# Optimization experiments

Hardware: AMD Instinct MI355X
Metric: run time of the kernel (lower is better)

## Reference

```python
import jax, jax.numpy as jnp
import numpy as np

D_MODEL = 1024
NUM_HEADS = 16
D_HEAD = D_MODEL // NUM_HEADS


def setup_inputs() -> dict:
    key = jax.random.key(0)
    ks = jax.random.split(key, 12)
    B, S = 4, 2048
    scale = 1.0 / np.sqrt(D_MODEL)
    inp = {
        "query": jax.random.normal(ks[0], (B, S, D_MODEL), dtype=jnp.float32),
        "key": jax.random.normal(ks[1], (B, S, D_MODEL), dtype=jnp.float32),
        "value": jax.random.normal(ks[2], (B, S, D_MODEL), dtype=jnp.float32),
        "Wq": jax.random.normal(ks[3], (D_MODEL, D_MODEL), dtype=jnp.float32) * scale,
        "bq": jnp.zeros((D_MODEL,), dtype=jnp.float32),
        "Wk": jax.random.normal(ks[4], (D_MODEL, D_MODEL), dtype=jnp.float32) * scale,
        "bk": jnp.zeros((D_MODEL,), dtype=jnp.float32),
        "Wv": jax.random.normal(ks[5], (D_MODEL, D_MODEL), dtype=jnp.float32) * scale,
        "bv": jnp.zeros((D_MODEL,), dtype=jnp.float32),
        "Wo": jax.random.normal(ks[6], (D_MODEL, D_MODEL), dtype=jnp.float32) * scale,
        "bo": jnp.zeros((D_MODEL,), dtype=jnp.float32),
    }
    return inp


def reference(query, key, value, Wq, bq, Wk, bk, Wv, bv, Wo, bo):
    B, S, _ = query.shape
    # Linear projections (torch Linear: x @ W.T + b), split into heads: [B, H, S, Dh]
    Q = (query @ Wq.T + bq).reshape(B, S, NUM_HEADS, D_HEAD).transpose(0, 2, 1, 3)
    K = (key @ Wk.T + bk).reshape(B, S, NUM_HEADS, D_HEAD).transpose(0, 2, 1, 3)
    V = (value @ Wv.T + bv).reshape(B, S, NUM_HEADS, D_HEAD).transpose(0, 2, 1, 3)
    scores = jnp.einsum("bhqd,bhkd->bhqk", Q, K) / np.sqrt(D_HEAD).astype(np.float32)
    attn = jax.nn.softmax(scores, axis=-1)  # dropout is identity in eval mode
    out = jnp.einsum("bhqk,bhkd->bhqd", attn, V)
    out = out.transpose(0, 2, 1, 3).reshape(B, S, D_MODEL)
    out = out @ Wo.T + bo
    avg_attention = attn.mean(axis=1)  # [B, S, S]
    return (out, avg_attention)
```

## Files before the change

### kernel.cpp

```cpp
#include <hip/hip_runtime.h>
#include <hip/hip_bf16.h>


#define DEVI __device__ __forceinline__

typedef __attribute__((ext_vector_type(8))) short bf16x8;
typedef __attribute__((ext_vector_type(4))) float f32x4;

#define MFMA_BF16(a, b, c) __builtin_amdgcn_mfma_f32_16x16x32_bf16(a, b, c, 0, 0, 0)

constexpr int Bn = 4;
constexpr int Sn = 2048;
constexpr int Dn = 1024;
constexpr int Hn = 16;

DEVI unsigned short f2bf_rn(float x) {
    unsigned u = __float_as_uint(x);
    u += 0x7fffu + ((u >> 16) & 1u);
    return (unsigned short)(u >> 16);
}
DEVI float bf2f(unsigned short h) { return __uint_as_float(((unsigned)h) << 16); }

DEVI int swz32(int r, int k) { return r * 32 + ((((k >> 3) ^ r) & 3) << 3) + (k & 7); }
DEVI int swz64(int r, int k) { return r * 64 + ((((k >> 3) ^ r) & 7) << 3) + (k & 7); }

DEVI void gload16(const unsigned short* g, unsigned short* l) {
    __builtin_amdgcn_global_load_lds(
        (const __attribute__((address_space(1))) unsigned int*)g,
        (__attribute__((address_space(3))) unsigned int*)l, 16, 0, 0);
}

__global__ __launch_bounds__(256) void cvt_plain3(
    const float* __restrict__ a, const float* __restrict__ b, const float* __restrict__ c,
    unsigned short* __restrict__ oa, unsigned short* __restrict__ ob,
    unsigned short* __restrict__ oc)
{
    const float* s = blockIdx.y == 0 ? a : blockIdx.y == 1 ? b : c;
    unsigned short* d = blockIdx.y == 0 ? oa : blockIdx.y == 1 ? ob : oc;
    const size_t i = ((size_t)blockIdx.x * 256 + threadIdx.x) * 8;
    const float4 v0 = *reinterpret_cast<const float4*>(s + i);
    const float4 v1 = *reinterpret_cast<const float4*>(s + i + 4);
    const float* p0 = reinterpret_cast<const float*>(&v0);
    const float* p1 = reinterpret_cast<const float*>(&v1);
    bf16x8 o;
#pragma unroll
    for (int j = 0; j < 4; ++j) {
        o[j] = (short)f2bf_rn(p0[j]);
        o[4 + j] = (short)f2bf_rn(p1[j]);
    }
    *reinterpret_cast<bf16x8*>(d + i) = o;
}

__global__ __launch_bounds__(256) void cvt_split4(
    const float* __restrict__ w0, const float* __restrict__ w1,
    const float* __restrict__ w2, const float* __restrict__ w3,
    unsigned short* __restrict__ h0, unsigned short* __restrict__ l0,
    unsigned short* __restrict__ h1, unsigned short* __restrict__ l1,
    unsigned short* __restrict__ h2, unsigned short* __restrict__ l2,
    unsigned short* __restrict__ h3, unsigned short* __restrict__ l3)
{
    const int y = blockIdx.y;
    const float* s = y == 0 ? w0 : y == 1 ? w1 : y == 2 ? w2 : w3;
    unsigned short* dh = y == 0 ? h0 : y == 1 ? h1 : y == 2 ? h2 : h3;
    unsigned short* dl = y == 0 ? l0 : y == 1 ? l1 : y == 2 ? l2 : l3;
    const size_t i = ((size_t)blockIdx.x * 256 + threadIdx.x) * 8;
    const float4 v0 = *reinterpret_cast<const float4*>(s + i);
    const float4 v1 = *reinterpret_cast<const float4*>(s + i + 4);
    const float* p0 = reinterpret_cast<const float*>(&v0);
    const float* p1 = reinterpret_cast<const float*>(&v1);
    bf16x8 oh, ol;
#pragma unroll
    for (int j = 0; j < 4; ++j) {
        unsigned short h = f2bf_rn(p0[j]);
        oh[j] = (short)h;
        ol[j] = (short)f2bf_rn(p0[j] - bf2f(h));
        h = f2bf_rn(p1[j]);
        oh[4 + j] = (short)h;
        ol[4 + j] = (short)f2bf_rn(p1[j] - bf2f(h));
    }
    *reinterpret_cast<bf16x8*>(dh + i) = oh;
    *reinterpret_cast<bf16x8*>(dl + i) = ol;
}

template <int MODE>
__global__ __launch_bounds__(256) void gemm_bf(
    const unsigned short* __restrict__ Xbf,
    const unsigned short* __restrict__ Whi, const unsigned short* __restrict__ Wlo,
    const float* __restrict__ bias, float oscale,
    unsigned short* __restrict__ o_bf, float* __restrict__ o_f32)
{
    constexpr int K = Dn;
    __shared__ __align__(16) unsigned short sA[128 * 32];
    __shared__ __align__(16) unsigned short sBh[128 * 32];
    __shared__ __align__(16) unsigned short sBl[128 * 32];

    const int tid = threadIdx.x, lane = tid & 63, w = tid >> 6;
    const int row0 = blockIdx.y * 128, col0 = blockIdx.x * 128;
    const int wm = (w >> 1) * 64, wn = (w & 1) * 64;
    const int fr = lane & 15, hi = lane >> 4, kof = hi * 8;

    const int g0 = tid, g1 = tid + 256;
    const int r0 = g0 >> 2, c0 = ((g0 & 3) ^ r0) & 3;
    const int r1 = g1 >> 2, c1 = ((g1 & 3) ^ r1) & 3;

    const unsigned short* pa0 = Xbf + (size_t)(row0 + r0) * K + c0 * 8;
    const unsigned short* pa1 = Xbf + (size_t)(row0 + r1) * K + c1 * 8;
    const unsigned short* pbh0 = Whi + (size_t)(col0 + r0) * K + c0 * 8;
    const unsigned short* pbh1 = Whi + (size_t)(col0 + r1) * K + c1 * 8;
    const unsigned short* pbl0 = Wlo + (size_t)(col0 + r0) * K + c0 * 8;
    const unsigned short* pbl1 = Wlo + (size_t)(col0 + r1) * K + c1 * 8;

    f32x4 acc[4][4] = {};

    for (int k0 = 0; k0 < K; k0 += 32) {
        gload16(pa0 + k0, &sA[(w * 64) * 8]);
        gload16(pa1 + k0, &sA[(256 + w * 64) * 8]);
        gload16(pbh0 + k0, &sBh[(w * 64) * 8]);
        gload16(pbh1 + k0, &sBh[(256 + w * 64) * 8]);
        gload16(pbl0 + k0, &sBl[(w * 64) * 8]);
        gload16(pbl1 + k0, &sBl[(256 + w * 64) * 8]);
        __syncthreads();

        bf16x8 fa[4], fbh[4], fbl[4];
#pragma unroll
        for (int m = 0; m < 4; ++m) fa[m] = *(const bf16x8*)&sA[swz32(wm + m * 16 + fr, kof)];
#pragma unroll
        for (int n = 0; n < 4; ++n) {
            const int ib = swz32(wn + n * 16 + fr, kof);
            fbh[n] = *(const bf16x8*)&sBh[ib];
            fbl[n] = *(const bf16x8*)&sBl[ib];
        }
#pragma unroll
        for (int m = 0; m < 4; ++m)
#pragma unroll
            for (int n = 0; n < 4; ++n) {
                acc[m][n] = MFMA_BF16(fa[m], fbh[n], acc[m][n]);
                acc[m][n] = MFMA_BF16(fa[m], fbl[n], acc[m][n]);
            }
        __syncthreads();
    }

    float bv_[4];
#pragma unroll
    for (int n = 0; n < 4; ++n) bv_[n] = bias[col0 + wn + n * 16 + fr];

#pragma unroll
    for (int m = 0; m < 4; ++m)
#pragma unroll
        for (int n = 0; n < 4; ++n)
#pragma unroll
            for (int r = 0; r < 4; ++r) {
                const int row = row0 + wm + m * 16 + hi * 4 + r;
                const int col = col0 + wn + n * 16 + fr;
                float v = acc[m][n][r] + bv_[n];
                if (MODE == 0) {
                    v *= oscale;
                    const int bb = row >> 11, s = row & 2047;
                    const int hh = col >> 6, dh = col & 63;
                    o_bf[((size_t)(bb * Hn + hh) * Sn + s) * 64 + dh] = f2bf_rn(v);
                } else if (MODE == 1) {
                    const int bb = row >> 11, s = row & 2047;
                    const int hh = col >> 6, dh = col & 63;
                    o_bf[((size_t)(bb * Hn + hh) * 64 + dh) * Sn + s] = f2bf_rn(v);
                } else {
                    o_f32[(size_t)row * Dn + col] = v;
                }
            }
}

__global__ __launch_bounds__(256) void flash_fwd(
    const unsigned short* __restrict__ Qbf, const unsigned short* __restrict__ Kbf,
    const unsigned short* __restrict__ Vt,
    unsigned short* __restrict__ attn_bf, float* __restrict__ m_ws, float* __restrict__ l_ws)
{
    __shared__ __align__(16) unsigned short kh_l[2][64 * 64];
    __shared__ __align__(16) unsigned short vt_l[2][64 * 64];
    __shared__ __align__(16) unsigned short p_l[4 * 16 * 64];

    const int tid = threadIdx.x, lane = tid & 63, w = tid >> 6;
    const int qt = blockIdx.x & 31;
    const int h = (blockIdx.x >> 5) & 15;
    const int b = blockIdx.x >> 9;
    const int fr = lane & 15, kof = (lane >> 4) * 8;
    const size_t head = (size_t)(b * Hn + h) * Sn;
    const int qbase = qt * 64;
    const int qrow = qbase + w * 16 + fr;

    const int gS0 = w * 64 + lane, gS1 = 256 + w * 64 + lane;
    const int rS0 = gS0 >> 3, cS0 = ((gS0 & 7) ^ rS0) & 7;
    const int rS1 = gS1 >> 3, cS1 = ((gS1 & 7) ^ rS1) & 7;
    const unsigned short* kp0 = Kbf + (head + rS0) * 64 + cS0 * 8;
    const unsigned short* kp1 = Kbf + (head + rS1) * 64 + cS1 * 8;
    const unsigned short* vp0 = Vt + ((size_t)(b * Hn + h) * 64 + rS0) * Sn + cS0 * 8;
    const unsigned short* vp1 = Vt + ((size_t)(b * Hn + h) * 64 + rS1) * Sn + cS1 * 8;

    bf16x8 aq[2];
    {
        const unsigned short* qp = Qbf + (head + qrow) * 64;
        aq[0] = *(const bf16x8*)(qp + kof);
        aq[1] = *(const bf16x8*)(qp + 32 + kof);
    }

    float m_r[4] = {-1e30f, -1e30f, -1e30f, -1e30f};
    float l_r[4] = {0.f, 0.f, 0.f, 0.f};
    f32x4 o[4] = {};
    int cur = 0;

    gload16(kp0, &kh_l[0][(w * 64) * 8]);
    gload16(kp1, &kh_l[0][(256 + w * 64) * 8]);
    gload16(vp0, &vt_l[0][(w * 64) * 8]);
    gload16(vp1, &vt_l[0][(256 + w * 64) * 8]);
    __syncthreads();

    for (int kb = 0; kb < Sn; kb += 64) {
        if (kb + 64 < Sn) {
            const int nb = cur ^ 1;
            gload16(kp0 + (size_t)(kb + 64) * 64, &kh_l[nb][(w * 64) * 8]);
            gload16(kp1 + (size_t)(kb + 64) * 64, &kh_l[nb][(256 + w * 64) * 8]);
            gload16(vp0 + kb + 64, &vt_l[nb][(w * 64) * 8]);
            gload16(vp1 + kb + 64, &vt_l[nb][(256 + w * 64) * 8]);
        }

        f32x4 sc[4] = {};
#pragma unroll
        for (int n = 0; n < 4; ++n) {
            const int kr = n * 16 + fr;
#pragma unroll
            for (int ks = 0; ks < 2; ++ks) {
                const bf16x8 bh = *(const bf16x8*)&kh_l[cur][swz64(kr, ks * 32 + kof)];
                sc[n] = MFMA_BF16(aq[ks], bh, sc[n]);
            }
        }

        float mnew[4];
        bool grow = false;
#pragma unroll
        for (int r = 0; r < 4; ++r) {
            float rm = fmaxf(fmaxf(sc[0][r], sc[1][r]), fmaxf(sc[2][r], sc[3][r]));
            rm = fmaxf(rm, __shfl_xor(rm, 1));
            rm = fmaxf(rm, __shfl_xor(rm, 2));
            rm = fmaxf(rm, __shfl_xor(rm, 4));
            rm = fmaxf(rm, __shfl_xor(rm, 8));
            mnew[r] = fmaxf(m_r[r], rm);
            grow = grow || (mnew[r] > m_r[r]);
        }
        if (__any((int)grow)) {
#pragma unroll
            for (int r = 0; r < 4; ++r) {
                const float scale_ = __builtin_amdgcn_exp2f(m_r[r] - mnew[r]);
#pragma unroll
                for (int n = 0; n < 4; ++n) o[n][r] *= scale_;
                l_r[r] *= scale_;
                m_r[r] = mnew[r];
            }
        }

        float rsum[4] = {0.f, 0.f, 0.f, 0.f};
#pragma unroll
        for (int n = 0; n < 4; ++n)
#pragma unroll
            for (int r = 0; r < 4; ++r) {
                const float p = __builtin_amdgcn_exp2f(sc[n][r] - m_r[r]);
                rsum[r] += p;
                p_l[w * 1024 + swz64((lane >> 4) * 4 + r, n * 16 + fr)] = f2bf_rn(p);
            }
#pragma unroll
        for (int r = 0; r < 4; ++r) {
            float t = rsum[r];
            t += __shfl_xor(t, 1);
            t += __shfl_xor(t, 2);
            t += __shfl_xor(t, 4);
            t += __shfl_xor(t, 8);
            l_r[r] += t;
        }

        const bf16x8 pa0 = *(const bf16x8*)&p_l[w * 1024 + swz64(fr, kof)];
        const bf16x8 pa1 = *(const bf16x8*)&p_l[w * 1024 + swz64(fr, 32 + kof)];
#pragma unroll
        for (int n = 0; n < 4; ++n) {
            const bf16x8 bv0 = *(const bf16x8*)&vt_l[cur][swz64(n * 16 + fr, kof)];
            const bf16x8 bv1 = *(const bf16x8*)&vt_l[cur][swz64(n * 16 + fr, 32 + kof)];
            o[n] = MFMA_BF16(pa0, bv0, o[n]);
            o[n] = MFMA_BF16(pa1, bv1, o[n]);
        }
        __syncthreads();
        cur ^= 1;
    }

#pragma unroll
    for (int r = 0; r < 4; ++r) {
        const float inv = 1.f / l_r[r];
        const int row_ = qbase + w * 16 + (lane >> 4) * 4 + r;
#pragma unroll
        for (int n = 0; n < 4; ++n)
            attn_bf[((size_t)(b * Sn + row_)) * Dn + h * 64 + n * 16 + fr] =
                f2bf_rn(o[n][r] * inv);
    }
    if (fr == 0) {
#pragma unroll
        for (int r = 0; r < 4; ++r) {
            const int row_ = qbase + w * 16 + (lane >> 4) * 4 + r;
            m_ws[head + row_] = m_r[r];
            l_ws[head + row_] = l_r[r];
        }
    }
}

__global__ __launch_bounds__(256) void avg_attn_kernel(
    const unsigned short* __restrict__ Qbf, const unsigned short* __restrict__ Kbf,
    const float* __restrict__ m_ws, const float* __restrict__ l_ws,
    float* __restrict__ avg)
{
    __shared__ __align__(16) unsigned short kh_l[64 * 64];

    const int tid = threadIdx.x, lane = tid & 63, w = tid >> 6;
    const int kt = blockIdx.x & 31;
    const int qt = (blockIdx.x >> 5) & 31;
    const int b = blockIdx.x >> 10;
    const int fr = lane & 15, kof = (lane >> 4) * 8;
    const int qbase = qt * 64, kbase = kt * 64;
    const int qrow = qbase + w * 16 + fr;

    const int gS0 = w * 64 + lane, gS1 = 256 + w * 64 + lane;
    const int rS0 = gS0 >> 3, cS0 = ((gS0 & 7) ^ rS0) & 7;
    const int rS1 = gS1 >> 3, cS1 = ((gS1 & 7) ^ rS1) & 7;

    f32x4 facc[4] = {};

    for (int h = 0; h < Hn; ++h) {
        const size_t head = (size_t)(b * Hn + h) * Sn;
        gload16(Kbf + (head + kbase + rS0) * 64 + cS0 * 8, &kh_l[(w * 64) * 8]);
        gload16(Kbf + (head + kbase + rS1) * 64 + cS1 * 8, &kh_l[(256 + w * 64) * 8]);
        __syncthreads();

        const unsigned short* qp = Qbf + (head + qrow) * 64;
        const bf16x8 aq0 = *(const bf16x8*)(qp + kof);
        const bf16x8 aq1 = *(const bf16x8*)(qp + 32 + kof);

        f32x4 sc[4] = {};
#pragma unroll
        for (int n = 0; n < 4; ++n) {
            const int kr = n * 16 + fr;
            const bf16x8 bh0 = *(const bf16x8*)&kh_l[swz64(kr, kof)];
            const bf16x8 bh1 = *(const bf16x8*)&kh_l[swz64(kr, 32 + kof)];
            sc[n] = MFMA_BF16(aq0, bh0, sc[n]);
            sc[n] = MFMA_BF16(aq1, bh1, sc[n]);
        }
#pragma unroll
        for (int r = 0; r < 4; ++r) {
            const int row_ = qbase + w * 16 + (lane >> 4) * 4 + r;
            const float mm = m_ws[head + row_];
            const float li = 0.0625f / l_ws[head + row_];
#pragma unroll
            for (int n = 0; n < 4; ++n)
                facc[n][r] += __builtin_amdgcn_exp2f(sc[n][r] - mm) * li;
        }
        __syncthreads();
    }

#pragma unroll
    for (int r = 0; r < 4; ++r) {
        const int row_ = qbase + w * 16 + (lane >> 4) * 4 + r;
#pragma unroll
        for (int n = 0; n < 4; ++n)
            avg[((size_t)(b * Sn + row_)) * Sn + kbase + n * 16 + fr] = facc[n][r];
    }
}

extern "C" void kernel_launch(void* const* d_in, const int* in_sizes, int n_in,
                              void* d_out, int out_size, void* d_ws, size_t ws_size,
                              hipStream_t stream)
{
    const float* query = (const float*)d_in[0];
    const float* key_ = (const float*)d_in[1];
    const float* value = (const float*)d_in[2];
    const float* Wq = (const float*)d_in[3];
    const float* bq = (const float*)d_in[4];
    const float* Wk = (const float*)d_in[5];
    const float* bk = (const float*)d_in[6];
    const float* Wv = (const float*)d_in[7];
    const float* bv = (const float*)d_in[8];
    const float* Wo = (const float*)d_in[9];
    const float* bo = (const float*)d_in[10];

    const size_t QE = (size_t)Bn * Hn * Sn * 64;
    const size_t WE = (size_t)Dn * Dn;

    unsigned short* Qbf = (unsigned short*)d_ws;
    unsigned short* Kbf = Qbf + QE;
    unsigned short* Vt = Kbf + QE;
    unsigned short* Xq = Vt + QE;
    unsigned short* Xk = Xq + QE;
    unsigned short* Xv = Xk + QE;
    unsigned short* Wqh = Xv + QE;
    unsigned short* Wql = Wqh + WE;
    unsigned short* Wkh = Wql + WE;
    unsigned short* Wkl = Wkh + WE;
    unsigned short* Wvh = Wkl + WE;
    unsigned short* Wvl = Wvh + WE;
    unsigned short* Woh = Wvl + WE;
    unsigned short* Wol = Woh + WE;
    float* m_ws = (float*)(Wol + WE);
    float* l_ws = m_ws + (size_t)Bn * Hn * Sn;
    unsigned short* attn_bf = Xq;

    float* out0 = (float*)d_out;
    float* avg = out0 + (size_t)Bn * Sn * Dn;

    const float QSC = 0.125f * 1.44269504088896341f;

    cvt_plain3<<<dim3(4096, 3), 256, 0, stream>>>(query, key_, value, Xq, Xk, Xv);
    cvt_split4<<<dim3(512, 4), 256, 0, stream>>>(Wq, Wk, Wv, Wo, Wqh, Wql, Wkh, Wkl,
                                                 Wvh, Wvl, Woh, Wol);

    const dim3 gg(8, 64), bb(256);
    gemm_bf<0><<<gg, bb, 0, stream>>>(Xq, Wqh, Wql, bq, QSC, Qbf, nullptr);
    gemm_bf<0><<<gg, bb, 0, stream>>>(Xk, Wkh, Wkl, bk, 1.0f, Kbf, nullptr);
    gemm_bf<1><<<gg, bb, 0, stream>>>(Xv, Wvh, Wvl, bv, 1.0f, Vt, nullptr);
    flash_fwd<<<dim3(Bn * Hn * (Sn / 64)), bb, 0, stream>>>(Qbf, Kbf, Vt, attn_bf,
                                                            m_ws, l_ws);
    avg_attn_kernel<<<dim3(Bn * 32 * 32), bb, 0, stream>>>(Qbf, Kbf, m_ws, l_ws, avg);
    gemm_bf<2><<<gg, bb, 0, stream>>>(attn_bf, Woh, Wol, bo, 1.0f, nullptr, out0);
}
```

Before: 662.8 us.

## Lazy softmax max rescaling, deferred row-sum reduction, and double-buffered K in avg kernel

The flash attention loop now starts from a fixed max threshold of 8. It does the cross-lane max reduction and rescale only when some lane's local max exceeds the current running max. The row-sum shuffle reduction moves out of the loop, so each lane keeps a partial sum and reduces once at the end. The avg-attention kernel double-buffers K tiles across heads, prefetching the next head while computing the current one. The fixed threshold assumes scaled scores stay near 8 and risks overflow or precision loss if they exceed that range a lot.

```diff
diff --git a/kernel.cpp b/kernel.cpp
--- a/kernel.cpp
+++ b/kernel.cpp
@@ -201,8 +201,8 @@
         aq[1] = *(const bf16x8*)(qp + 32 + kof);
     }
 
-    float m_r[4] = {-1e30f, -1e30f, -1e30f, -1e30f};
-    float l_r[4] = {0.f, 0.f, 0.f, 0.f};
+    float m_r[4] = {8.0f, 8.0f, 8.0f, 8.0f};
+    float lp[4] = {0.f, 0.f, 0.f, 0.f};
     f32x4 o[4] = {};
     int cur = 0;
 
@@ -232,47 +232,37 @@
             }
         }
 
-        float mnew[4];
         bool grow = false;
 #pragma unroll
         for (int r = 0; r < 4; ++r) {
-            float rm = fmaxf(fmaxf(sc[0][r], sc[1][r]), fmaxf(sc[2][r], sc[3][r]));
-            rm = fmaxf(rm, __shfl_xor(rm, 1));
-            rm = fmaxf(rm, __shfl_xor(rm, 2));
-            rm = fmaxf(rm, __shfl_xor(rm, 4));
-            rm = fmaxf(rm, __shfl_xor(rm, 8));
-            mnew[r] = fmaxf(m_r[r], rm);
-            grow = grow || (mnew[r] > m_r[r]);
+            const float lm = fmaxf(fmaxf(sc[0][r], sc[1][r]), fmaxf(sc[2][r], sc[3][r]));
+            grow = grow || (lm > m_r[r]);
         }
         if (__any((int)grow)) {
 #pragma unroll
             for (int r = 0; r < 4; ++r) {
-                const float scale_ = __builtin_amdgcn_exp2f(m_r[r] - mnew[r]);
-#pragma unroll
-                for (int n = 0; n < 4; ++n) o[n][r] *= scale_;
-                l_r[r] *= scale_;
-                m_r[r] = mnew[r];
+                float rm = fmaxf(fmaxf(sc[0][r], sc[1][r]), fmaxf(sc[2][r], sc[3][r]));
+                rm = fmaxf(rm, __shfl_xor(rm, 1));
+                rm = fmaxf(rm, __shfl_xor(rm, 2));
+                rm = fmaxf(rm, __shfl_xor(rm, 4));
+                rm = fmaxf(rm, __shfl_xor(rm, 8));
+                const float mn = fmaxf(m_r[r], rm);
+                const float sf = __builtin_amdgcn_exp2f(m_r[r] - mn);
+#pragma unroll
+                for (int n = 0; n < 4; ++n) o[n][r] *= sf;
+                lp[r] *= sf;
+                m_r[r] = mn;
             }
         }
 
-        float rsum[4] = {0.f, 0.f, 0.f, 0.f};
 #pragma unroll
         for (int n = 0; n < 4; ++n)
 #pragma unroll
             for (int r = 0; r < 4; ++r) {
                 const float p = __builtin_amdgcn_exp2f(sc[n][r] - m_r[r]);
-                rsum[r] += p;
+                lp[r] += p;
                 p_l[w * 1024 + swz64((lane >> 4) * 4 + r, n * 16 + fr)] = f2bf_rn(p);
             }
-#pragma unroll
-        for (int r = 0; r < 4; ++r) {
-            float t = rsum[r];
-            t += __shfl_xor(t, 1);
-            t += __shfl_xor(t, 2);
-            t += __shfl_xor(t, 4);
-            t += __shfl_xor(t, 8);
-            l_r[r] += t;
-        }
 
         const bf16x8 pa0 = *(const bf16x8*)&p_l[w * 1024 + swz64(fr, kof)];
         const bf16x8 pa1 = *(const bf16x8*)&p_l[w * 1024 + swz64(fr, 32 + kof)];
@@ -287,6 +277,17 @@
         cur ^= 1;
     }
 
+    float l_r[4];
+#pragma unroll
+    for (int r = 0; r < 4; ++r) {
+        float t = lp[r];
+        t += __shfl_xor(t, 1);
+        t += __shfl_xor(t, 2);
+        t += __shfl_xor(t, 4);
+        t += __shfl_xor(t, 8);
+        l_r[r] = t;
+    }
+
 #pragma unroll
     for (int r = 0; r < 4; ++r) {
         const float inv = 1.f / l_r[r];
@@ -311,7 +312,7 @@
     const float* __restrict__ m_ws, const float* __restrict__ l_ws,
     float* __restrict__ avg)
 {
-    __shared__ __align__(16) unsigned short kh_l[64 * 64];
+    __shared__ __align__(16) unsigned short kh_l[2][64 * 64];
 
     const int tid = threadIdx.x, lane = tid & 63, w = tid >> 6;
     const int kt = blockIdx.x & 31;
@@ -326,13 +327,23 @@
     const int rS1 = gS1 >> 3, cS1 = ((gS1 & 7) ^ rS1) & 7;
 
     f32x4 facc[4] = {};
+    int cur = 0;
+
+    {
+        const size_t hd = (size_t)(b * Hn) * Sn;
+        gload16(Kbf + (hd + kbase + rS0) * 64 + cS0 * 8, &kh_l[0][(w * 64) * 8]);
+        gload16(Kbf + (hd + kbase + rS1) * 64 + cS1 * 8, &kh_l[0][(256 + w * 64) * 8]);
+    }
+    __syncthreads();
 
     for (int h = 0; h < Hn; ++h) {
+        if (h + 1 < Hn) {
+            const size_t hd = (size_t)(b * Hn + h + 1) * Sn;
+            const int nb = cur ^ 1;
+            gload16(Kbf + (hd + kbase + rS0) * 64 + cS0 * 8, &kh_l[nb][(w * 64) * 8]);
+            gload16(Kbf + (hd + kbase + rS1) * 64 + cS1 * 8, &kh_l[nb][(256 + w * 64) * 8]);
+        }
         const size_t head = (size_t)(b * Hn + h) * Sn;
-        gload16(Kbf + (head + kbase + rS0) * 64 + cS0 * 8, &kh_l[(w * 64) * 8]);
-        gload16(Kbf + (head + kbase + rS1) * 64 + cS1 * 8, &kh_l[(256 + w * 64) * 8]);
-        __syncthreads();
-
         const unsigned short* qp = Qbf + (head + qrow) * 64;
         const bf16x8 aq0 = *(const bf16x8*)(qp + kof);
         const bf16x8 aq1 = *(const bf16x8*)(qp + 32 + kof);
@@ -341,8 +352,8 @@
 #pragma unroll
         for (int n = 0; n < 4; ++n) {
             const int kr = n * 16 + fr;
-            const bf16x8 bh0 = *(const bf16x8*)&kh_l[swz64(kr, kof)];
-            const bf16x8 bh1 = *(const bf16x8*)&kh_l[swz64(kr, 32 + kof)];
+            const bf16x8 bh0 = *(const bf16x8*)&kh_l[cur][swz64(kr, kof)];
+            const bf16x8 bh1 = *(const bf16x8*)&kh_l[cur][swz64(kr, 32 + kof)];
             sc[n] = MFMA_BF16(aq0, bh0, sc[n]);
             sc[n] = MFMA_BF16(aq1, bh1, sc[n]);
         }
@@ -356,6 +367,7 @@
                 facc[n][r] += __builtin_amdgcn_exp2f(sc[n][r] - mm) * li;
         }
         __syncthreads();
+        cur ^= 1;
     }
 
 #pragma unroll
```

Result: faster. 604.5 us (-8.8%).
